# Kernel tuning notes

Measured on AMD Instinct MI355X. Metric: run time of the kernel, lower is better.

The kernel has to match this reference:

```python
import jax, jax.numpy as jnp
import numpy as np

N = 16384
E = 524288
IN_DIM = 128
LATENT = 48
EPS = 1e-5


def setup_inputs() -> dict:
    key = jax.random.key(0)
    ks = jax.random.split(key, 20)
    def rn(k, shape, scale=0.05):
        return jax.random.normal(k, shape, dtype=jnp.float32) * scale
    return {
        "x": jax.random.normal(ks[0], (N, IN_DIM), dtype=jnp.float32),
        "edge_index": jax.random.randint(ks[1], (2, E), 0, N, dtype=jnp.int64),
        "W1": rn(ks[2], (IN_DIM, 256)), "b1": jnp.zeros((256,), jnp.float32),
        "W2": rn(ks[3], (256, 128)),    "b2": jnp.zeros((128,), jnp.float32),
        "W3": rn(ks[4], (128, LATENT)), "b3": jnp.zeros((LATENT,), jnp.float32),
        "skip_W": rn(ks[5], (IN_DIM, LATENT)), "skip_b": jnp.zeros((LATENT,), jnp.float32),
        "bn_gamma": jnp.ones((256,), jnp.float32), "bn_beta": jnp.zeros((256,), jnp.float32),
        "bn_mean": rn(ks[6], (256,), 0.01), "bn_var": jnp.ones((256,), jnp.float32),
        "dpW1": rn(ks[7], (LATENT, 64)), "dpb1": jnp.zeros((64,), jnp.float32),
        "dpW2": rn(ks[8], (64, 1)),      "dpb2": jnp.zeros((1,), jnp.float32),
    }


def _gcn_norm(edge_index, n):
    # add self-loops, compute symmetric normalization (PyG gcn_norm)
    loops = jnp.arange(n, dtype=edge_index.dtype)
    src = jnp.concatenate([edge_index[0], loops])
    dst = jnp.concatenate([edge_index[1], loops])
    deg = jax.ops.segment_sum(jnp.ones_like(dst, dtype=jnp.float32), dst, num_segments=n)
    dinv = jnp.where(deg > 0, jax.lax.rsqrt(jnp.maximum(deg, 1.0)), 0.0)
    norm = dinv[src] * dinv[dst]  # [E+N]
    return src, dst, norm


def _gcn_conv(x, src, dst, norm, W, b, n):
    h = x @ W                                    # [N, out]
    msg = h[src] * norm[:, None]                 # gather + scale, [E+N, out]
    return jax.ops.segment_sum(msg, dst, num_segments=n) + b


def reference(x, edge_index, W1, b1, W2, b2, W3, b3, skip_W, skip_b,
              bn_gamma, bn_beta, bn_mean, bn_var, dpW1, dpb1, dpW2, dpb2):
    n = x.shape[0]
    src, dst, norm = _gcn_norm(edge_index, n)
    identity = x @ skip_W + skip_b
    h = _gcn_conv(x, src, dst, norm, W1, b1, n)
    # BatchNorm1d (inference mode: running stats), then ReLU; dropout = identity (eval)
    h = (h - bn_mean) * jax.lax.rsqrt(bn_var + EPS) * bn_gamma + bn_beta
    h = jax.nn.relu(h)
    h = jax.nn.relu(_gcn_conv(h, src, dst, norm, W2, b2, n))
    z = _gcn_conv(h, src, dst, norm, W3, b3, n) + identity   # [N, latent]
    adj_recon = jax.nn.sigmoid(z @ z.T)                      # [N, N]
    degree_pred = (jax.nn.relu(z @ dpW1 + dpb1) @ dpW2 + dpb2).squeeze(-1)
    return z, adj_recon, degree_pred
```

## Files before the change

kernel.cpp:

```cpp
#include <hip/hip_runtime.h>
#include <hip/hip_bf16.h>
#include <math.h>

#define NN   16384
#define EE   524288
#define TOTE (EE + NN)
#define CAP  128

typedef short s16x8 __attribute__((ext_vector_type(8)));
typedef float f32x16 __attribute__((ext_vector_type(16)));

__device__ inline unsigned short bf16r(float f) {
    unsigned int u = __float_as_uint(f);
    return (unsigned short)((u + 0x7FFFu + ((u >> 16) & 1u)) >> 16);
}

__global__ void k_prep(const float* __restrict__ x,  const float* __restrict__ W1,
                       const float* __restrict__ W2, const float* __restrict__ W3,
                       const float* __restrict__ skW,
                       const float* __restrict__ b1, const float* __restrict__ gamma,
                       const float* __restrict__ beta, const float* __restrict__ mean,
                       const float* __restrict__ var,  const int* __restrict__ ei,
                       unsigned short* __restrict__ xb,  unsigned short* __restrict__ W1t,
                       unsigned short* __restrict__ W2t, unsigned short* __restrict__ W3t,
                       unsigned short* __restrict__ skWt,
                       float* __restrict__ bnA, float* __restrict__ bnC,
                       int* __restrict__ cur, int* __restrict__ cs) {
    const int S0 = NN * 128;
    const int S1 = S0 + 256 * 128;
    const int S2 = S1 + 128 * 256;
    const int S3 = S2 + 64 * 128;
    const int S4 = S3 + 64 * 128;
    int i = blockIdx.x * 256 + threadIdx.x;
    if (i < TOTE) {
        int s, d;
        if (i < EE) { s = ei[i]; d = ei[EE + i]; }
        else        { s = d = i - EE; }
        int pos = atomicAdd(&cur[d], 1);
        if (pos < CAP) cs[(d << 7) + pos] = s;
    }
    if (i < S0) { xb[i] = bf16r(x[i]); }
    else if (i < S1) { int j = i - S0; int n = j >> 7, k = j & 127; W1t[j] = bf16r(W1[k * 256 + n]); }
    else if (i < S2) { int j = i - S1; int n = j >> 8, k = j & 255; W2t[j] = bf16r(W2[k * 128 + n]); }
    else if (i < S3) { int j = i - S2; int n = j >> 7, k = j & 127; W3t[j] = (n < 48) ? bf16r(W3[k * 48 + n]) : 0; }
    else if (i < S4) { int j = i - S3; int n = j >> 7, k = j & 127; skWt[j] = (n < 48) ? bf16r(skW[k * 48 + n]) : 0; }
    else if (i < S4 + 256) {
        int j = i - S4;
        float a = gamma[j] * rsqrtf(var[j] + 1e-5f);
        bnA[j] = a;
        bnC[j] = (b1[j] - mean[j]) * a + beta[j];
    }
}

__global__ void k_xbs(const float* __restrict__ x, const int* __restrict__ cur,
                      float* __restrict__ dinv, unsigned short* __restrict__ xbs) {
    int i = blockIdx.x * 256 + threadIdx.x;
    if (i < NN) dinv[i] = rsqrtf((float)cur[i]);
    xbs[i] = bf16r(x[i] * rsqrtf((float)cur[i >> 7]));
}

template <int MODE>
__global__ void k_agg128(const unsigned short* __restrict__ H, const int* __restrict__ cur,
                         const int* __restrict__ cs, const float* __restrict__ dinv,
                         const float* __restrict__ bias, unsigned short* __restrict__ Y) {
    int node = blockIdx.x * 4 + (threadIdx.x >> 6);
    int lane = threadIdx.x & 63;
    int cnt = cur[node]; if (cnt > CAP) cnt = CAP;
    int s0 = node << 7;
    const unsigned int* Hp = (const unsigned int*)H;
    float ax = 0.f, ay = 0.f;
    for (int base = 0; base < cnt; base += 64) {
        int nb = cnt - base; if (nb > 64) nb = 64;
        int vi = (lane < nb) ? cs[s0 + base + lane] : 0;
        int e = 0;
        for (; e + 8 <= nb; e += 8) {
            unsigned int u[8];
#pragma unroll
            for (int q = 0; q < 8; q++) {
                int iq = __shfl(vi, e + q);
                u[q] = Hp[(size_t)iq * 64 + lane];
            }
#pragma unroll
            for (int q = 0; q < 8; q++) {
                ax += __uint_as_float(u[q] << 16);
                ay += __uint_as_float(u[q] & 0xffff0000u);
            }
        }
        for (; e < nb; e++) {
            int iq = __shfl(vi, e);
            unsigned int u0 = Hp[(size_t)iq * 64 + lane];
            ax += __uint_as_float(u0 << 16);
            ay += __uint_as_float(u0 & 0xffff0000u);
        }
    }
    float dn = dinv[node];
    ax *= dn; ay *= dn;
    if constexpr (MODE == 2) {
        ax = fmaxf(ax + bias[2 * lane], 0.f);
        ay = fmaxf(ay + bias[2 * lane + 1], 0.f);
    }
    unsigned int o = ((unsigned int)bf16r(ay) << 16) | bf16r(ax);
    ((unsigned int*)Y)[(size_t)node * 64 + lane] = o;
}

__global__ void k_aggz(const unsigned short* __restrict__ H, const int* __restrict__ cur,
                       const int* __restrict__ cs, const float* __restrict__ dinv,
                       const float* __restrict__ b3, const float* __restrict__ idb,
                       const float* __restrict__ dpW1, const float* __restrict__ dpb1,
                       const float* __restrict__ dpW2, const float* __restrict__ dpb2,
                       float* __restrict__ zout, unsigned short* __restrict__ zb,
                       float* __restrict__ dpout) {
    int node = blockIdx.x * 4 + (threadIdx.x >> 6);
    int lane = threadIdx.x & 63;
    int cnt = cur[node]; if (cnt > CAP) cnt = CAP;
    int s0 = node << 7;
    float a = 0.f;
    for (int base = 0; base < cnt; base += 64) {
        int nb = cnt - base; if (nb > 64) nb = 64;
        int vi = (lane < nb) ? cs[s0 + base + lane] : 0;
        int e = 0;
        for (; e + 8 <= nb; e += 8) {
            float v[8];
#pragma unroll
            for (int q = 0; q < 8; q++) {
                int iq = __shfl(vi, e + q);
                v[q] = __uint_as_float((unsigned int)H[(size_t)iq * 64 + lane] << 16);
            }
#pragma unroll
            for (int q = 0; q < 8; q++) a += v[q];
        }
        for (; e < nb; e++) {
            int iq = __shfl(vi, e);
            a += __uint_as_float((unsigned int)H[(size_t)iq * 64 + lane] << 16);
        }
    }
    float zv = 0.f;
    if (lane < 48) {
        zv = a * dinv[node] + b3[lane] + idb[(size_t)node * 64 + lane];
        zout[(size_t)node * 48 + lane] = zv;
        zb[(size_t)node * 48 + lane] = bf16r(zv);
    }
    float hj = dpb1[lane];
#pragma unroll
    for (int k = 0; k < 48; k++) hj += __shfl(zv, k) * dpW1[k * 64 + lane];
    hj = fmaxf(hj, 0.f);
    float p = hj * dpW2[lane];
    for (int o = 32; o > 0; o >>= 1) p += __shfl_down(p, o);
    if (lane == 0) dpout[node] = p + dpb2[0];
}

template <int K, int NP, int MODE, int TW>
__global__ void k_mm(const unsigned short* __restrict__ A,
                     const unsigned short* __restrict__ Bt,
                     const float* __restrict__ P0, const float* __restrict__ P1,
                     const float* __restrict__ RS,
                     void* __restrict__ Yv) {
    int wv = threadIdx.x >> 6, l = threadIdx.x & 63;
    int ti = blockIdx.x;
    int tj = blockIdx.y * TW + wv;
    int r = l & 31, hi = l >> 5;
    const s16x8* ap = (const s16x8*)(A + (size_t)(ti * 32 + r) * K + 8 * hi);
    const s16x8* bp = (const s16x8*)(Bt + (size_t)(tj * 32 + r) * K + 8 * hi);
    f32x16 c = {};
#pragma unroll
    for (int kk = 0; kk < K / 16; kk++)
        c = __builtin_amdgcn_mfma_f32_32x32x16_bf16(ap[2 * kk], bp[2 * kk], c, 0, 0, 0);
    int col = tj * 32 + r;
#pragma unroll
    for (int reg = 0; reg < 16; reg++) {
        int row = ti * 32 + (reg & 3) + 8 * (reg >> 2) + 4 * hi;
        float v = c[reg];
        if constexpr (MODE == 1) {
            v = fmaxf(v * P0[col] + P1[col], 0.f);
            ((unsigned short*)Yv)[(size_t)row * NP + col] = bf16r(v);
        } else {
            ((unsigned short*)Yv)[(size_t)row * NP + col] = bf16r(v * RS[row]);
        }
    }
}

__global__ void k_mm3s(const unsigned short* __restrict__ h2a,
                       const unsigned short* __restrict__ W3t,
                       const unsigned short* __restrict__ xb,
                       const unsigned short* __restrict__ skWt,
                       const float* __restrict__ skb, const float* __restrict__ dinv,
                       unsigned short* __restrict__ h3b, float* __restrict__ idb) {
    int wv = threadIdx.x >> 6, l = threadIdx.x & 63;
    int ti = blockIdx.x;
    int tj = wv;
    int r = l & 31, hi = l >> 5;
    const unsigned short* A  = (blockIdx.y == 0) ? h2a : xb;
    const unsigned short* Bt = (blockIdx.y == 0) ? W3t : skWt;
    const s16x8* ap = (const s16x8*)(A + (size_t)(ti * 32 + r) * 128 + 8 * hi);
    const s16x8* bp = (const s16x8*)(Bt + (size_t)(tj * 32 + r) * 128 + 8 * hi);
    f32x16 c = {};
#pragma unroll
    for (int kk = 0; kk < 8; kk++)
        c = __builtin_amdgcn_mfma_f32_32x32x16_bf16(ap[2 * kk], bp[2 * kk], c, 0, 0, 0);
    int col = tj * 32 + r;
    if (blockIdx.y == 0) {
#pragma unroll
        for (int reg = 0; reg < 16; reg++) {
            int row = ti * 32 + (reg & 3) + 8 * (reg >> 2) + 4 * hi;
            h3b[(size_t)row * 64 + col] = bf16r(c[reg] * dinv[row]);
        }
    } else {
        float add = (col < 48) ? skb[col] : 0.f;
#pragma unroll
        for (int reg = 0; reg < 16; reg++) {
            int row = ti * 32 + (reg & 3) + 8 * (reg >> 2) + 4 * hi;
            idb[(size_t)row * 64 + col] = c[reg] + add;
        }
    }
}

__global__ __launch_bounds__(256) void k_adj2(const unsigned short* __restrict__ zb,
                                              float* __restrict__ out) {
    int wv = threadIdx.x >> 6;
    int l  = threadIdx.x & 63;
    int ti = blockIdx.y;
    int tj = blockIdx.x * 4 + wv;
    int r  = l & 31;
    int hi = l >> 5;

    const s16x8* ap = (const s16x8*)(zb + (size_t)(ti * 32 + r) * 48 + 8 * hi);
    const s16x8* bp = (const s16x8*)(zb + (size_t)(tj * 32 + r) * 48 + 8 * hi);

    f32x16 c = {};
#pragma unroll
    for (int kk = 0; kk < 3; kk++) {
        s16x8 a = ap[2 * kk];
        s16x8 b = bp[2 * kk];
        c = __builtin_amdgcn_mfma_f32_32x32x16_bf16(a, b, c, 0, 0, 0);
    }

    size_t colbase = (size_t)tj * 32 + r;
#pragma unroll
    for (int reg = 0; reg < 16; reg++) {
        int row = ti * 32 + (reg & 3) + 8 * (reg >> 2) + 4 * hi;
        float v = 1.f / (1.f + __expf(-c[reg]));
        __builtin_nontemporal_store(v, out + (size_t)row * NN + colbase);
    }
}

extern "C" void kernel_launch(void* const* d_in, const int* in_sizes, int n_in,
                              void* d_out, int out_size, void* d_ws, size_t ws_size,
                              hipStream_t stream) {
    const float* x      = (const float*)d_in[0];
    const int*   ei     = (const int*)d_in[1];
    const float* W1     = (const float*)d_in[2];
    const float* b1     = (const float*)d_in[3];
    const float* W2     = (const float*)d_in[4];
    const float* b2     = (const float*)d_in[5];
    const float* W3     = (const float*)d_in[6];
    const float* b3     = (const float*)d_in[7];
    const float* skW    = (const float*)d_in[8];
    const float* skb    = (const float*)d_in[9];
    const float* gamma  = (const float*)d_in[10];
    const float* beta   = (const float*)d_in[11];
    const float* mean   = (const float*)d_in[12];
    const float* var    = (const float*)d_in[13];
    const float* dpW1   = (const float*)d_in[14];
    const float* dpb1   = (const float*)d_in[15];
    const float* dpW2   = (const float*)d_in[16];
    const float* dpb2   = (const float*)d_in[17];

    float* zout   = (float*)d_out;
    float* adjout = zout + (size_t)NN * 48;
    float* dpout  = adjout + (size_t)NN * NN;

    char* w = (char*)d_ws;
    auto alloc = [&](size_t bytes) {
        char* p = w; w += ((bytes + 255) & ~(size_t)255); return p;
    };
    int*   cur  = (int*)alloc((size_t)NN * 4);
    int*   cs   = (int*)alloc((size_t)NN * CAP * 4);
    float* dinv = (float*)alloc((size_t)NN * 4);
    float* bnA  = (float*)alloc(256 * 4);
    float* bnC  = (float*)alloc(256 * 4);
    unsigned short* xb   = (unsigned short*)alloc((size_t)NN * 128 * 2);
    unsigned short* xbs  = (unsigned short*)alloc((size_t)NN * 128 * 2);
    unsigned short* W1t  = (unsigned short*)alloc(256 * 128 * 2);
    unsigned short* W2t  = (unsigned short*)alloc(128 * 256 * 2);
    unsigned short* W3t  = (unsigned short*)alloc(64 * 128 * 2);
    unsigned short* skWt = (unsigned short*)alloc(64 * 128 * 2);
    unsigned short* xa   = (unsigned short*)alloc((size_t)NN * 128 * 2);
    unsigned short* h1   = (unsigned short*)alloc((size_t)NN * 256 * 2);
    unsigned short* h2   = (unsigned short*)alloc((size_t)NN * 128 * 2);
    unsigned short* h2a  = (unsigned short*)alloc((size_t)NN * 128 * 2);
    unsigned short* h3b  = (unsigned short*)alloc((size_t)NN * 64 * 2);
    float* idb  = (float*)alloc((size_t)NN * 64 * 4);
    unsigned short* zb = (unsigned short*)alloc((size_t)NN * 48 * 2);

    hipMemsetAsync(cur, 0, (size_t)NN * 4, stream);

    const int PREP = NN * 128 + 256 * 128 + 128 * 256 + 64 * 128 + 64 * 128 + 256;
    k_prep<<<(PREP + 255) / 256, 256, 0, stream>>>(x, W1, W2, W3, skW,
                                                   b1, gamma, beta, mean, var, ei,
                                                   xb, W1t, W2t, W3t, skWt,
                                                   bnA, bnC, cur, cs);
    k_xbs<<<NN * 128 / 256, 256, 0, stream>>>(x, cur, dinv, xbs);

    k_agg128<0><<<NN / 4, 256, 0, stream>>>(xbs, cur, cs, dinv, nullptr, xa);
    k_mm<128, 256, 1, 4><<<dim3(NN / 32, 2), 256, 0, stream>>>(xa, W1t, bnA, bnC, nullptr, h1);
    k_mm<256, 128, 4, 4><<<dim3(NN / 32, 1), 256, 0, stream>>>(h1, W2t, nullptr, nullptr, dinv, h2);
    k_agg128<2><<<NN / 4, 256, 0, stream>>>(h2, cur, cs, dinv, b2, h2a);
    k_mm3s<<<dim3(NN / 32, 2), 128, 0, stream>>>(h2a, W3t, xb, skWt, skb, dinv, h3b, idb);
    k_aggz<<<NN / 4, 256, 0, stream>>>(h3b, cur, cs, dinv, b3, idb,
                                       dpW1, dpb1, dpW2, dpb2, zout, zb, dpout);

    k_adj2<<<dim3(128, 512), 256, 0, stream>>>(zb, adjout);
}
```

Baseline: 291.1 us.

## Fuse first aggregation and two GEMMs into one shared-memory encoder kernel

Replaces the first sparse aggregation kernel and the two following MFMA GEMM kernels with a single kernel per 32-node tile. It aggregates neighbours into LDS, runs the W1 GEMM with BN+ReLU into LDS, then the W2 GEMM scaled by dinv, writing only h2 to global memory. This removes the global round-trips of the xa and h1 intermediates and two launches. In exchange, each 512-thread block does serial gather work before its GEMM phases, with only half the waves active in the second GEMM, which may reduce occupancy and latency hiding.

After: 282.0 us. 3.1% less time.

```diff
diff --git a/kernel.cpp b/kernel.cpp
--- a/kernel.cpp
+++ b/kernel.cpp
@@ -59,6 +59,93 @@
     xbs[i] = bf16r(x[i] * rsqrtf((float)cur[i >> 7]));
 }
 
+__global__ __launch_bounds__(512) void k_enc1(
+        const unsigned short* __restrict__ xbs, const int* __restrict__ cur,
+        const int* __restrict__ cs, const float* __restrict__ dinv,
+        const unsigned short* __restrict__ W1t, const unsigned short* __restrict__ W2t,
+        const float* __restrict__ bnA, const float* __restrict__ bnC,
+        unsigned short* __restrict__ h2) {
+    __shared__ unsigned int   xs[32][68];
+    __shared__ unsigned short h1s[32][264];
+    int tid = threadIdx.x;
+    int wv = tid >> 6, l = tid & 63;
+    int nb0 = blockIdx.x * 32;
+    const unsigned int* Hp = (const unsigned int*)xbs;
+
+    for (int it = 0; it < 4; it++) {
+        int lr = wv * 4 + it;
+        int node = nb0 + lr;
+        int cnt = cur[node]; if (cnt > CAP) cnt = CAP;
+        int s0 = node << 7;
+        float ax = 0.f, ay = 0.f;
+        for (int base = 0; base < cnt; base += 64) {
+            int nbv = cnt - base; if (nbv > 64) nbv = 64;
+            int vi = (l < nbv) ? cs[s0 + base + l] : 0;
+            int e = 0;
+            for (; e + 8 <= nbv; e += 8) {
+                unsigned int u[8];
+#pragma unroll
+                for (int q = 0; q < 8; q++) {
+                    int iq = __shfl(vi, e + q);
+                    u[q] = Hp[(size_t)iq * 64 + l];
+                }
+#pragma unroll
+                for (int q = 0; q < 8; q++) {
+                    ax += __uint_as_float(u[q] << 16);
+                    ay += __uint_as_float(u[q] & 0xffff0000u);
+                }
+            }
+            for (; e < nbv; e++) {
+                int iq = __shfl(vi, e);
+                unsigned int u0 = Hp[(size_t)iq * 64 + l];
+                ax += __uint_as_float(u0 << 16);
+                ay += __uint_as_float(u0 & 0xffff0000u);
+            }
+        }
+        float dn = dinv[node];
+        ax *= dn; ay *= dn;
+        xs[lr][l] = ((unsigned int)bf16r(ay) << 16) | bf16r(ax);
+    }
+    __syncthreads();
+
+    {
+        int r = l & 31, hi = l >> 5, tj = wv;
+        const s16x8* bp = (const s16x8*)(W1t + (size_t)(tj * 32 + r) * 128 + 8 * hi);
+        f32x16 c = {};
+#pragma unroll
+        for (int kk = 0; kk < 8; kk++) {
+            s16x8 a = *(const s16x8*)((const unsigned short*)&xs[r][0] + 16 * kk + 8 * hi);
+            c = __builtin_amdgcn_mfma_f32_32x32x16_bf16(a, bp[2 * kk], c, 0, 0, 0);
+        }
+        int col = tj * 32 + r;
+        float A0 = bnA[col], C0 = bnC[col];
+#pragma unroll
+        for (int reg = 0; reg < 16; reg++) {
+            int row = (reg & 3) + 8 * (reg >> 2) + 4 * hi;
+            h1s[row][col] = bf16r(fmaxf(c[reg] * A0 + C0, 0.f));
+        }
+    }
+    __syncthreads();
+
+    if (wv < 4) {
+        int r = l & 31, hi = l >> 5, tj = wv;
+        const s16x8* bp = (const s16x8*)(W2t + (size_t)(tj * 32 + r) * 256 + 8 * hi);
+        f32x16 c = {};
+#pragma unroll
+        for (int kk = 0; kk < 16; kk++) {
+            s16x8 a = *(const s16x8*)(&h1s[r][16 * kk + 8 * hi]);
+            c = __builtin_amdgcn_mfma_f32_32x32x16_bf16(a, bp[2 * kk], c, 0, 0, 0);
+        }
+        int col = tj * 32 + r;
+#pragma unroll
+        for (int reg = 0; reg < 16; reg++) {
+            int row = (reg & 3) + 8 * (reg >> 2) + 4 * hi;
+            int grow = nb0 + row;
+            h2[(size_t)grow * 128 + col] = bf16r(c[reg] * dinv[grow]);
+        }
+    }
+}
+
 template <int MODE>
 __global__ void k_agg128(const unsigned short* __restrict__ H, const int* __restrict__ cur,
                          const int* __restrict__ cs, const float* __restrict__ dinv,
@@ -147,36 +234,6 @@
     float p = hj * dpW2[lane];
     for (int o = 32; o > 0; o >>= 1) p += __shfl_down(p, o);
     if (lane == 0) dpout[node] = p + dpb2[0];
-}
-
-template <int K, int NP, int MODE, int TW>
-__global__ void k_mm(const unsigned short* __restrict__ A,
-                     const unsigned short* __restrict__ Bt,
-                     const float* __restrict__ P0, const float* __restrict__ P1,
-                     const float* __restrict__ RS,
-                     void* __restrict__ Yv) {
-    int wv = threadIdx.x >> 6, l = threadIdx.x & 63;
-    int ti = blockIdx.x;
-    int tj = blockIdx.y * TW + wv;
-    int r = l & 31, hi = l >> 5;
-    const s16x8* ap = (const s16x8*)(A + (size_t)(ti * 32 + r) * K + 8 * hi);
-    const s16x8* bp = (const s16x8*)(Bt + (size_t)(tj * 32 + r) * K + 8 * hi);
-    f32x16 c = {};
-#pragma unroll
-    for (int kk = 0; kk < K / 16; kk++)
-        c = __builtin_amdgcn_mfma_f32_32x32x16_bf16(ap[2 * kk], bp[2 * kk], c, 0, 0, 0);
-    int col = tj * 32 + r;
-#pragma unroll
-    for (int reg = 0; reg < 16; reg++) {
-        int row = ti * 32 + (reg & 3) + 8 * (reg >> 2) + 4 * hi;
-        float v = c[reg];
-        if constexpr (MODE == 1) {
-            v = fmaxf(v * P0[col] + P1[col], 0.f);
-            ((unsigned short*)Yv)[(size_t)row * NP + col] = bf16r(v);
-        } else {
-            ((unsigned short*)Yv)[(size_t)row * NP + col] = bf16r(v * RS[row]);
-        }
-    }
 }
 
 __global__ void k_mm3s(const unsigned short* __restrict__ h2a,
@@ -284,8 +341,6 @@
     unsigned short* W2t  = (unsigned short*)alloc(128 * 256 * 2);
     unsigned short* W3t  = (unsigned short*)alloc(64 * 128 * 2);
     unsigned short* skWt = (unsigned short*)alloc(64 * 128 * 2);
-    unsigned short* xa   = (unsigned short*)alloc((size_t)NN * 128 * 2);
-    unsigned short* h1   = (unsigned short*)alloc((size_t)NN * 256 * 2);
     unsigned short* h2   = (unsigned short*)alloc((size_t)NN * 128 * 2);
     unsigned short* h2a  = (unsigned short*)alloc((size_t)NN * 128 * 2);
     unsigned short* h3b  = (unsigned short*)alloc((size_t)NN * 64 * 2);
@@ -301,9 +356,7 @@
                                                    bnA, bnC, cur, cs);
     k_xbs<<<NN * 128 / 256, 256, 0, stream>>>(x, cur, dinv, xbs);
 
-    k_agg128<0><<<NN / 4, 256, 0, stream>>>(xbs, cur, cs, dinv, nullptr, xa);
-    k_mm<128, 256, 1, 4><<<dim3(NN / 32, 2), 256, 0, stream>>>(xa, W1t, bnA, bnC, nullptr, h1);
-    k_mm<256, 128, 4, 4><<<dim3(NN / 32, 1), 256, 0, stream>>>(h1, W2t, nullptr, nullptr, dinv, h2);
+    k_enc1<<<NN / 32, 512, 0, stream>>>(xbs, cur, cs, dinv, W1t, W2t, bnA, bnC, h2);
     k_agg128<2><<<NN / 4, 256, 0, stream>>>(h2, cur, cs, dinv, b2, h2a);
     k_mm3s<<<dim3(NN / 32, 2), 128, 0, stream>>>(h2a, W3t, xb, skWt, skb, dinv, h3b, idb);
     k_aggz<<<NN / 4, 256, 0, stream>>>(h3b, cur, cs, dinv, b3, idb,
```
